# Optimization experiments

Measured on AMD Instinct MI355X. Metric: run time of the kernel, lower is better.

The kernel has to match this reference:

```python
import jax, jax.numpy as jnp
import numpy as np

D_MODEL = 512
HEADS = 8
FF_HIDDEN = 1024
EPS = 1e-6


def setup_inputs() -> dict:
    key = jax.random.key(0)
    ks = jax.random.split(key, 12)
    s = 1.0 / np.sqrt(D_MODEL)
    inp = {
        'x': jax.random.normal(ks[0], (2, 4096, D_MODEL), dtype=jnp.float32),
        'Wq': jax.random.normal(ks[1], (D_MODEL, D_MODEL), dtype=jnp.float32) * s,
        'bq': jnp.zeros((D_MODEL,), jnp.float32),
        'Wk': jax.random.normal(ks[2], (D_MODEL, D_MODEL), dtype=jnp.float32) * s,
        'bk': jnp.zeros((D_MODEL,), jnp.float32),
        'Wv': jax.random.normal(ks[3], (D_MODEL, D_MODEL), dtype=jnp.float32) * s,
        'bv': jnp.zeros((D_MODEL,), jnp.float32),
        'Wo': jax.random.normal(ks[4], (D_MODEL, D_MODEL), dtype=jnp.float32) * s,
        'bo': jnp.zeros((D_MODEL,), jnp.float32),
        'a1': jnp.ones((D_MODEL,), jnp.float32),
        'b1': jnp.zeros((D_MODEL,), jnp.float32),
        'a2': jnp.ones((D_MODEL,), jnp.float32),
        'b2': jnp.zeros((D_MODEL,), jnp.float32),
        'W1': jax.random.normal(ks[5], (D_MODEL, FF_HIDDEN), dtype=jnp.float32) * s,
        'c1': jnp.zeros((FF_HIDDEN,), jnp.float32),
        'W2': jax.random.normal(ks[6], (FF_HIDDEN, D_MODEL), dtype=jnp.float32) * (1.0 / np.sqrt(FF_HIDDEN)),
        'c2': jnp.zeros((D_MODEL,), jnp.float32),
    }
    return inp


def _layer_norm(x, a, b):
    # Faithful to source: uses unbiased std (torch default) and divides by (std + eps)
    mean = jnp.mean(x, axis=-1, keepdims=True)
    std = jnp.std(x, axis=-1, keepdims=True, ddof=1)
    return a * ((x - mean) / (std + EPS)) + b


def _encoder_block(x, Wq, bq, Wk, bk, Wv, bv, Wo, bo, a1, b1, a2, b2, W1, c1, W2, c2):
    B, S, D = x.shape
    H, dk = HEADS, D // HEADS
    q = (x @ Wq + bq).reshape(B, S, H, dk).transpose(0, 2, 1, 3)  # [B,H,S,dk]
    k = (x @ Wk + bk).reshape(B, S, H, dk).transpose(0, 2, 1, 3)
    v = (x @ Wv + bv).reshape(B, S, H, dk).transpose(0, 2, 1, 3)
    scores = jnp.einsum('bhqd,bhkd->bhqk', q, k) / np.sqrt(dk)
    probs = jax.nn.softmax(scores, axis=-1)
    attn = jnp.einsum('bhqk,bhkd->bhqd', probs, v)
    concat = attn.transpose(0, 2, 1, 3).reshape(B, S, D)
    attn_out = concat @ Wo + bo
    x = _layer_norm(x + attn_out, a1, b1)  # dropout = identity (eval mode)
    ffn = jax.nn.relu(x @ W1 + c1) @ W2 + c2
    return _layer_norm(x + ffn, a2, b2)


def reference(x, Wq, bq, Wk, bk, Wv, bv, Wo, bo, a1, b1, a2, b2, W1, c1, W2, c2):
    return _encoder_block(x, Wq, bq, Wk, bk, Wv, bv, Wo, bo, a1, b1, a2, b2, W1, c1, W2, c2)
```

## Files before the change

### kernel.cpp

```cpp
#include <hip/hip_runtime.h>
#include <stdint.h>

typedef short short8 __attribute__((ext_vector_type(8)));
typedef short short4v __attribute__((ext_vector_type(4)));
typedef float f32x4 __attribute__((ext_vector_type(4)));
typedef float f32x16 __attribute__((ext_vector_type(16)));
typedef unsigned int u32x4 __attribute__((ext_vector_type(4)));

#define LOG2E 1.44269504088896f
#define QSCALE (0.125f * LOG2E)

__device__ __forceinline__ unsigned short f2b(float f) {
  union { float f; unsigned int u; } x; x.f = f;
  unsigned int u = x.u;
  unsigned int r = (u + 0x7fffu + ((u >> 16) & 1u)) >> 16;
  return (unsigned short)r;
}
__device__ __forceinline__ float b2f(unsigned short s) {
  union { unsigned int u; float f; } x; x.u = ((unsigned int)s) << 16;
  return x.f;
}
__device__ __forceinline__ void gl16(const void* g, void* l) {
  __builtin_amdgcn_global_load_lds((const __attribute__((address_space(1))) void*)g,
                                   (__attribute__((address_space(3))) void*)l, 16, 0, 0);
}
__device__ __forceinline__ unsigned int cvtpk(float lo, float hi) {
  unsigned int r;
  asm("v_cvt_pk_bf16_f32 %0, %1, %2" : "=v"(r) : "v"(lo), "v"(hi));
  return r;
}
__device__ __forceinline__ void plswap(unsigned int& a, unsigned int& b) {
  asm volatile("v_permlane32_swap_b32 %0, %1" : "+v"(a), "+v"(b));
}

__global__ __launch_bounds__(256) void prep_k(
    const float* __restrict__ X, unsigned short* __restrict__ Xb,
    const float* __restrict__ Wq, const float* __restrict__ Wk,
    const float* __restrict__ Wv, const float* __restrict__ Wo,
    const float* __restrict__ W1, const float* __restrict__ W2,
    unsigned short* __restrict__ WqkvT, unsigned short* __restrict__ WoT,
    unsigned short* __restrict__ W1T, unsigned short* __restrict__ W2T,
    const float* __restrict__ bq, const float* __restrict__ bk,
    const float* __restrict__ bv, float* __restrict__ Bqkv) {
  __shared__ float t[64][65];
  int bid = blockIdx.x, tid = threadIdx.x;
  if (bid < 2048) {
    int i = bid * 256 + tid;
    const float* p = X + (size_t)i * 8;
    float4 a = *(const float4*)(p);
    float4 b = *(const float4*)(p + 4);
    short8 o;
    o[0] = (short)f2b(a.x); o[1] = (short)f2b(a.y);
    o[2] = (short)f2b(a.z); o[3] = (short)f2b(a.w);
    o[4] = (short)f2b(b.x); o[5] = (short)f2b(b.y);
    o[6] = (short)f2b(b.z); o[7] = (short)f2b(b.w);
    *(short8*)(Xb + (size_t)i * 8) = o;
    return;
  }
  if (bid == 2560) {
    for (int i = tid; i < 1536; i += 256) {
      float v = (i < 512) ? bq[i] * QSCALE : (i < 1024 ? bk[i - 512] : bv[i - 1024]);
      Bqkv[i] = v;
    }
    return;
  }
  int idx = bid - 2048;
  const float* W; unsigned short* WT; int K, N, kb, nb; float scale = 1.0f;
  if (idx < 256) {
    int sec = idx >> 6, local = idx & 63;
    K = 512; N = 512; kb = local >> 3; nb = local & 7;
    if (sec == 0) { W = Wq; WT = WqkvT; scale = QSCALE; }
    else if (sec == 1) { W = Wk; WT = WqkvT + 512 * 512; }
    else if (sec == 2) { W = Wv; WT = WqkvT + 2 * 512 * 512; }
    else { W = Wo; WT = WoT; }
  } else if (idx < 384) {
    int local = idx - 256; K = 512; N = 1024; kb = local >> 4; nb = local & 15;
    W = W1; WT = W1T;
  } else {
    int local = idx - 384; K = 1024; N = 512; kb = local >> 3; nb = local & 7;
    W = W2; WT = W2T;
  }
  int k0 = kb * 64, n0 = nb * 64;
  for (int i = tid; i < 4096; i += 256) {
    int r = i >> 6, c = i & 63;
    t[r][c] = W[(size_t)(k0 + r) * N + n0 + c];
  }
  __syncthreads();
  for (int i = tid; i < 4096; i += 256) {
    int r = i >> 6, c = i & 63;
    WT[(size_t)(n0 + r) * K + k0 + c] = f2b(t[c][r] * scale);
  }
}

template <int EPI>
__global__ __launch_bounds__(256) void gemm_bt(
    const unsigned short* __restrict__ A, const unsigned short* __restrict__ BT,
    const float* __restrict__ bias, float* __restrict__ Cf,
    unsigned short* __restrict__ Cb, int M, int N, int K) {
  __shared__ unsigned short As[128 * 32];
  __shared__ unsigned short Bs[128 * 32];
  int t = threadIdx.x, w = t >> 6, l = t & 63;
  int linb = blockIdx.x + gridDim.x * blockIdx.y;
  int q8 = (gridDim.x * gridDim.y) >> 3;
  int wk = (linb & 7) * q8 + (linb >> 3);
  int bm = wk / gridDim.y, bn = wk % gridDim.y;
  int wm = w >> 1, wn = w & 1;
  int g = l >> 4, ln = l & 15;
  f32x4 acc[4][4] = {};
  const unsigned short* Arow = A + (size_t)bm * 128 * K;
  const unsigned short* Brow = BT + (size_t)bn * 128 * K;
  int nk = K >> 5;
  for (int kt = 0; kt < nk; ++kt) {
    int k0 = kt * 32;
#pragma unroll
    for (int i = 0; i < 2; ++i) {
      int cl = i * 256 + t;
      int r = cl >> 2, c = cl & 3;
      char* ldsA = (char*)As + (size_t)(i * 256 + w * 64) * 16;
      char* ldsB = (char*)Bs + (size_t)(i * 256 + w * 64) * 16;
      gl16(Arow + (size_t)r * K + k0 + c * 8, ldsA);
      gl16(Brow + (size_t)r * K + k0 + c * 8, ldsB);
    }
    __syncthreads();
    short8 af[4], bf[4];
    int ko = g * 8;
#pragma unroll
    for (int i = 0; i < 4; ++i)
      af[i] = *(const short8*)&As[(wm * 64 + i * 16 + ln) * 32 + ko];
#pragma unroll
    for (int j = 0; j < 4; ++j)
      bf[j] = *(const short8*)&Bs[(wn * 64 + j * 16 + ln) * 32 + ko];
    __builtin_amdgcn_s_setprio(1);
#pragma unroll
    for (int i = 0; i < 4; ++i)
#pragma unroll
      for (int j = 0; j < 4; ++j)
        acc[i][j] = __builtin_amdgcn_mfma_f32_16x16x32_bf16(af[i], bf[j], acc[i][j], 0, 0, 0);
    __builtin_amdgcn_s_setprio(0);
    __syncthreads();
  }
#pragma unroll
  for (int i = 0; i < 4; ++i) {
    int row = bm * 128 + wm * 64 + i * 16 + g * 4;
#pragma unroll
    for (int j = 0; j < 4; ++j) {
      int col = bn * 128 + wn * 64 + j * 16 + ln;
      float bv = bias[col];
      float vv[4];
#pragma unroll
      for (int r = 0; r < 4; ++r) {
        float v = acc[i][j][r] + bv;
        if constexpr (EPI == 2) v = v > 0.f ? v : 0.f;
        vv[r] = v;
      }
      if constexpr (EPI == 3) {
        if (col < 1024) {
#pragma unroll
          for (int r = 0; r < 4; ++r)
            Cb[(size_t)(col >> 9) * 4194304 + (size_t)(row + r) * 512 + (col & 511)] = f2b(vv[r]);
        } else {
          short4v pk;
#pragma unroll
          for (int r = 0; r < 4; ++r) pk[r] = (short)f2b(vv[r]);
          *(short4v*)((unsigned short*)Cf +
                      (size_t)((row >> 12) * 512 + (col & 511)) * 4096 + (row & 4095)) = pk;
        }
      } else {
#pragma unroll
        for (int r = 0; r < 4; ++r)
          Cb[(size_t)(row + r) * N + col] = f2b(vv[r]);
      }
    }
  }
}

template <int AMODE, bool WB>
__global__ __launch_bounds__(512) void gemmln_k(
    const unsigned short* __restrict__ A, const unsigned short* __restrict__ BT,
    const float* __restrict__ bias, const float* __restrict__ X,
    const float* __restrict__ gamma, const float* __restrict__ beta,
    float* __restrict__ outf, unsigned short* __restrict__ outb,
    const unsigned short* __restrict__ Opart, const float* __restrict__ L,
    int K) {
  __shared__ unsigned short As[AMODE ? 32 * 520 : 32 * 32];
  __shared__ unsigned short Bs[512 * 32];
  __shared__ float stats[8][32][2];
  __shared__ float minv[32][2];
  __shared__ float sli[8][32];
  int tid = threadIdx.x, wv = tid >> 6, lane = tid & 63;
  int g = lane >> 4, ln = lane & 15;
  int bm = blockIdx.x;
  int row0 = bm * 32;
  f32x4 acc[2][4] = {};

  if constexpr (AMODE == 1) {
    int b = row0 >> 12;
    int q0 = row0 & 4095;
    if (tid < 256) {
      int h = tid >> 5, qq = tid & 31;
      int bh = b * 8 + h;
      float s = L[(size_t)bh * 4096 + q0 + qq] + L[(size_t)(16 + bh) * 4096 + q0 + qq];
      sli[h][qq] = 1.0f / s;
    }
    __syncthreads();
    int col = tid;
    int h = col >> 6, d = col & 63;
    int bh = b * 8 + h;
    const unsigned short* p0 = Opart + (size_t)bh * 262144 + (size_t)d * 4096 + q0;
    const unsigned short* p1 = Opart + (size_t)(16 + bh) * 262144 + (size_t)d * 4096 + q0;
#pragma unroll
    for (int i = 0; i < 4; ++i) {
      short8 a = *(const short8*)(p0 + i * 8);
      short8 c = *(const short8*)(p1 + i * 8);
#pragma unroll
      for (int j = 0; j < 8; ++j) {
        int qq = i * 8 + j;
        float s = (b2f((unsigned short)a[j]) + b2f((unsigned short)c[j])) * sli[h][qq];
        As[qq * 520 + col] = f2b(s);
      }
    }
    __syncthreads();
  }

  const unsigned short* Arow = (AMODE == 0) ? (A + (size_t)bm * 32 * K) : nullptr;
  int nk = K >> 5;
  for (int kt = 0; kt < nk; ++kt) {
    int k0 = kt * 32;
    if constexpr (AMODE == 0) {
      if (tid < 128) {
        int r = tid >> 2, c = tid & 3;
        gl16(Arow + (size_t)r * K + k0 + c * 8, (char*)As + tid * 16);
      }
    }
#pragma unroll
    for (int i = 0; i < 4; ++i) {
      int u = i * 512 + tid;
      int r = u >> 2, c = u & 3;
      gl16(BT + (size_t)r * K + k0 + c * 8, (char*)Bs + (size_t)u * 16);
    }
    __syncthreads();
    short8 af[2], bf[4];
#pragma unroll
    for (int i = 0; i < 2; ++i) {
      if constexpr (AMODE == 1)
        af[i] = *(const short8*)&As[(i * 16 + ln) * 520 + k0 + g * 8];
      else
        af[i] = *(const short8*)&As[(i * 16 + ln) * 32 + g * 8];
    }
#pragma unroll
    for (int j = 0; j < 4; ++j)
      bf[j] = *(const short8*)&Bs[(wv * 64 + j * 16 + ln) * 32 + g * 8];
    __builtin_amdgcn_s_setprio(1);
#pragma unroll
    for (int i = 0; i < 2; ++i)
#pragma unroll
      for (int j = 0; j < 4; ++j)
        acc[i][j] = __builtin_amdgcn_mfma_f32_16x16x32_bf16(af[i], bf[j], acc[i][j], 0, 0, 0);
    __builtin_amdgcn_s_setprio(0);
    __syncthreads();
  }
  float v[2][4][4];
  float ps[8], pss[8];
#pragma unroll
  for (int k = 0; k < 8; ++k) { ps[k] = 0.f; pss[k] = 0.f; }
#pragma unroll
  for (int i = 0; i < 2; ++i)
#pragma unroll
    for (int j = 0; j < 4; ++j) {
      int col = wv * 64 + j * 16 + ln;
      float bv = bias[col];
#pragma unroll
      for (int r = 0; r < 4; ++r) {
        int row = i * 16 + g * 4 + r;
        float t = acc[i][j][r] + bv + X[(size_t)(row0 + row) * 512 + col];
        v[i][j][r] = t;
        ps[i * 4 + r] += t; pss[i * 4 + r] += t * t;
      }
    }
#pragma unroll
  for (int off = 1; off < 16; off <<= 1) {
#pragma unroll
    for (int k = 0; k < 8; ++k) {
      ps[k] += __shfl_xor(ps[k], off);
      pss[k] += __shfl_xor(pss[k], off);
    }
  }
  if (ln == 0) {
#pragma unroll
    for (int i = 0; i < 2; ++i)
#pragma unroll
      for (int r = 0; r < 4; ++r) {
        stats[wv][i * 16 + g * 4 + r][0] = ps[i * 4 + r];
        stats[wv][i * 16 + g * 4 + r][1] = pss[i * 4 + r];
      }
  }
  __syncthreads();
  if (tid < 32) {
    float S = 0.f, SS = 0.f;
#pragma unroll
    for (int w2 = 0; w2 < 8; ++w2) { S += stats[w2][tid][0]; SS += stats[w2][tid][1]; }
    float mean = S * (1.f / 512.f);
    float var = fmaxf((SS - 512.f * mean * mean) * (1.f / 511.f), 0.f);
    minv[tid][0] = mean;
    minv[tid][1] = 1.f / (sqrtf(var) + 1e-6f);
  }
  __syncthreads();
#pragma unroll
  for (int i = 0; i < 2; ++i)
#pragma unroll
    for (int j = 0; j < 4; ++j) {
      int col = wv * 64 + j * 16 + ln;
      float gm = gamma[col], bt2 = beta[col];
#pragma unroll
      for (int r = 0; r < 4; ++r) {
        int row = i * 16 + g * 4 + r;
        float o = gm * ((v[i][j][r] - minv[row][0]) * minv[row][1]) + bt2;
        outf[(size_t)(row0 + row) * 512 + col] = o;
        if constexpr (WB) outb[(size_t)(row0 + row) * 512 + col] = f2b(o);
      }
    }
}

__global__ __launch_bounds__(256, 2) void attn_k(
    const unsigned short* __restrict__ Q, const unsigned short* __restrict__ Kb,
    const unsigned short* __restrict__ Vt, unsigned short* __restrict__ Opart,
    float* __restrict__ L) {
  __shared__ unsigned short Ks[2][4096];
  __shared__ unsigned short Vs[3][4096];
  int tid = threadIdx.x, wv = tid >> 6, lane = tid & 63;
  int l31 = lane & 31, hi = lane >> 5;
  int lin = blockIdx.x + 16 * blockIdx.y + 256 * blockIdx.z;
  int wk = (lin & 7) * 64 + (lin >> 3);
  int qb = wk & 15, bh = (wk >> 4) & 15, z = wk >> 8;
  int b = bh >> 3, h = bh & 7;
  int q0 = qb * 256 + wv * 64;
  int kvbase = z * 2048;

  short8 qfA[4], qfB[4];
  {
    const unsigned short* qpA = Q + (size_t)(b * 4096 + q0 + l31) * 512 + h * 64;
    const unsigned short* qpB = qpA + 32 * 512;
#pragma unroll
    for (int ks = 0; ks < 4; ++ks) {
      qfA[ks] = *(const short8*)(qpA + ks * 16 + hi * 8);
      qfB[ks] = *(const short8*)(qpB + ks * 16 + hi * 8);
    }
  }

  short8 ones;
#pragma unroll
  for (int j = 0; j < 8; ++j) ones[j] = (short)0x3F80;

  const f32x16 Z = {};
  f32x16 oA0 = {}, oA1 = {}, oB0 = {}, oB1 = {}, laccA = {}, laccB = {};

  int skk[2], sc[2];
#pragma unroll
  for (int i = 0; i < 2; ++i) {
    int u = i * 256 + tid;
    int r2 = u >> 4, s = u & 15;
    skk[i] = 2 * r2 + (s & 1);
    sc[i] = ((s >> 1) ^ (r2 & 7)) * 8;
  }

  auto stage = [&](char* kb_lds, char* vb_lds, int kv) {
    const unsigned short* ksrc = Kb + (size_t)(b * 4096 + kv) * 512 + h * 64;
    const unsigned short* vsrc = Vt + (size_t)(bh * 64) * 4096 + kv;
#pragma unroll
    for (int i = 0; i < 2; ++i) {
      gl16(ksrc + (size_t)skk[i] * 512 + sc[i], kb_lds + (size_t)(i * 256 + wv * 64) * 16);
      gl16(vsrc + (size_t)skk[i] * 4096 + sc[i], vb_lds + (size_t)(i * 256 + wv * 64) * 16);
    }
  };

  int r2a = l31 >> 1, par = l31 & 1, perm = r2a & 7;
  int rdb = r2a * 256 + (par << 4);

  auto qk = [&](const char* kbase, f32x16& sA0, f32x16& sA1, f32x16& sB0, f32x16& sB1) {
    __builtin_amdgcn_s_setprio(1);
#pragma unroll
    for (int ks = 0; ks < 4; ++ks) {
      int c16 = ks * 2 + hi;
      int byteA = rdb + (((c16 ^ perm) << 1) << 4);
      short8 k0 = *(const short8*)(kbase + byteA);
      short8 k1 = *(const short8*)(kbase + byteA + 4096);
      if (ks == 0) {
        sA0 = __builtin_amdgcn_mfma_f32_32x32x16_bf16(k0, qfA[0], Z, 0, 0, 0);
        sA1 = __builtin_amdgcn_mfma_f32_32x32x16_bf16(k1, qfA[0], Z, 0, 0, 0);
        sB0 = __builtin_amdgcn_mfma_f32_32x32x16_bf16(k0, qfB[0], Z, 0, 0, 0);
        sB1 = __builtin_amdgcn_mfma_f32_32x32x16_bf16(k1, qfB[0], Z, 0, 0, 0);
      } else {
        sA0 = __builtin_amdgcn_mfma_f32_32x32x16_bf16(k0, qfA[ks], sA0, 0, 0, 0);
        sA1 = __builtin_amdgcn_mfma_f32_32x32x16_bf16(k1, qfA[ks], sA1, 0, 0, 0);
        sB0 = __builtin_amdgcn_mfma_f32_32x32x16_bf16(k0, qfB[ks], sB0, 0, 0, 0);
        sB1 = __builtin_amdgcn_mfma_f32_32x32x16_bf16(k1, qfB[ks], sB1, 0, 0, 0);
      }
    }
    __builtin_amdgcn_s_setprio(0);
  };

  auto pv = [&](const char* vbase, const short8* pfA, const short8* pfB) {
    __builtin_amdgcn_s_setprio(1);
#pragma unroll
    for (int ks = 0; ks < 4; ++ks) {
      int c16 = ks * 2 + hi;
      int byteA = rdb + (((c16 ^ perm) << 1) << 4);
      short8 v0 = *(const short8*)(vbase + byteA);
      short8 v1 = *(const short8*)(vbase + byteA + 4096);
      oA0 = __builtin_amdgcn_mfma_f32_32x32x16_bf16(v0, pfA[ks], oA0, 0, 0, 0);
      oA1 = __builtin_amdgcn_mfma_f32_32x32x16_bf16(v1, pfA[ks], oA1, 0, 0, 0);
      oB0 = __builtin_amdgcn_mfma_f32_32x32x16_bf16(v0, pfB[ks], oB0, 0, 0, 0);
      oB1 = __builtin_amdgcn_mfma_f32_32x32x16_bf16(v1, pfB[ks], oB1, 0, 0, 0);
      laccA = __builtin_amdgcn_mfma_f32_32x32x16_bf16(ones, pfA[ks], laccA, 0, 0, 0);
      laccB = __builtin_amdgcn_mfma_f32_32x32x16_bf16(ones, pfB[ks], laccB, 0, 0, 0);
    }
    __builtin_amdgcn_s_setprio(0);
  };

  auto exppack = [&](f32x16& s0, f32x16& s1, short8* pf) {
#pragma unroll
    for (int r = 0; r < 16; ++r) s0[r] = __builtin_amdgcn_exp2f(s0[r]);
#pragma unroll
    for (int r = 0; r < 16; ++r) s1[r] = __builtin_amdgcn_exp2f(s1[r]);
    unsigned int u0 = cvtpk(s0[0], s0[1]), u1 = cvtpk(s0[4], s0[5]);
    plswap(u0, u1);
    unsigned int u2 = cvtpk(s0[2], s0[3]), u3 = cvtpk(s0[6], s0[7]);
    plswap(u2, u3);
    unsigned int u4 = cvtpk(s0[8], s0[9]), u5 = cvtpk(s0[12], s0[13]);
    plswap(u4, u5);
    unsigned int u6 = cvtpk(s0[10], s0[11]), u7 = cvtpk(s0[14], s0[15]);
    plswap(u6, u7);
    union { u32x4 u; short8 s; } cv;
    cv.u = (u32x4){u0, u2, u1, u3}; pf[0] = cv.s;
    cv.u = (u32x4){u4, u6, u5, u7}; pf[1] = cv.s;
    unsigned int w0 = cvtpk(s1[0], s1[1]), w1 = cvtpk(s1[4], s1[5]);
    plswap(w0, w1);
    unsigned int w2 = cvtpk(s1[2], s1[3]), w3 = cvtpk(s1[6], s1[7]);
    plswap(w2, w3);
    unsigned int w4 = cvtpk(s1[8], s1[9]), w5 = cvtpk(s1[12], s1[13]);
    plswap(w4, w5);
    unsigned int w6 = cvtpk(s1[10], s1[11]), w7 = cvtpk(s1[14], s1[15]);
    plswap(w6, w7);
    cv.u = (u32x4){w0, w2, w1, w3}; pf[2] = cv.s;
    cv.u = (u32x4){w4, w6, w5, w7}; pf[3] = cv.s;
  };

  char* k0b = (char*)&Ks[0][0];
  char* k1b = (char*)&Ks[1][0];
  char* vA = (char*)&Vs[0][0];
  char* vB = (char*)&Vs[1][0];
  char* vC = (char*)&Vs[2][0];
  stage(k0b, vA, kvbase);
  __syncthreads();
  stage(k1b, vB, kvbase + 64);

  f32x16 sA0, sA1, sB0, sB1;
  qk(k0b, sA0, sA1, sB0, sB1);
  short8 pfA[4], pfB[4];
  exppack(sA0, sA1, pfA);
  exppack(sB0, sB1, pfB);

#pragma unroll 1
  for (int t = 1; t < 32; ++t) {
    __syncthreads();
    char* kr = (t & 1) ? k1b : k0b;
    char* kw = (t & 1) ? k0b : k1b;
    if (t < 31) stage(kw, vC, kvbase + (t + 1) * 64);
    qk(kr, sA0, sA1, sB0, sB1);
    pv(vA, pfA, pfB);
    exppack(sA0, sA1, pfA);
    exppack(sB0, sB1, pfB);
    char* tmp = vA; vA = vB; vB = vC; vC = tmp;
  }
  pv(vA, pfA, pfB);

  int plane = z * 16 + bh;
  unsigned short* op = Opart + (size_t)plane * 262144;
  int qA = q0 + l31, qB = q0 + 32 + l31;
#pragma unroll
  for (int r = 0; r < 16; ++r) {
    int dr = (r & 3) + 8 * (r >> 2) + 4 * hi;
    op[(size_t)dr * 4096 + qA] = f2b(oA0[r]);
    op[(size_t)(dr + 32) * 4096 + qA] = f2b(oA1[r]);
    op[(size_t)dr * 4096 + qB] = f2b(oB0[r]);
    op[(size_t)(dr + 32) * 4096 + qB] = f2b(oB1[r]);
  }
  if (hi == 0) {
    L[(size_t)plane * 4096 + qA] = laccA[0];
    L[(size_t)plane * 4096 + qB] = laccB[0];
  }
}

extern "C" void kernel_launch(void* const* d_in, const int* in_sizes, int n_in,
                              void* d_out, int out_size, void* d_ws, size_t ws_size,
                              hipStream_t stream) {
  const float* x  = (const float*)d_in[0];
  const float* Wq = (const float*)d_in[1];
  const float* bq = (const float*)d_in[2];
  const float* Wk = (const float*)d_in[3];
  const float* bk = (const float*)d_in[4];
  const float* Wv = (const float*)d_in[5];
  const float* bv = (const float*)d_in[6];
  const float* Wo = (const float*)d_in[7];
  const float* bo = (const float*)d_in[8];
  const float* a1 = (const float*)d_in[9];
  const float* b1 = (const float*)d_in[10];
  const float* a2 = (const float*)d_in[11];
  const float* b2 = (const float*)d_in[12];
  const float* W1 = (const float*)d_in[13];
  const float* c1 = (const float*)d_in[14];
  const float* W2 = (const float*)d_in[15];
  const float* c2 = (const float*)d_in[16];

  char* ws = (char*)d_ws;
  const size_t MB = 1024 * 1024;
  unsigned short* Xb  = (unsigned short*)(ws + 0);
  unsigned short* Qb  = (unsigned short*)(ws + 8 * MB);
  unsigned short* Kbf = (unsigned short*)(ws + 16 * MB);
  float* L = (float*)(ws + 24 * MB);
  unsigned short* Vtb = (unsigned short*)(ws + 32 * MB);
  unsigned short* WqkvT = (unsigned short*)(ws + 40 * MB);
  unsigned short* WoT = (unsigned short*)(ws + 41 * MB + 512 * 1024);
  unsigned short* W1T = (unsigned short*)(ws + 42 * MB);
  unsigned short* W2T = (unsigned short*)(ws + 43 * MB);
  unsigned short* Opart = (unsigned short*)(ws + 44 * MB);
  float* Bqkv = (float*)(ws + 44 * MB);
  float* Y1 = (float*)(ws + 60 * MB);
  unsigned short* Y1b = Qb;
  unsigned short* Hb  = Kbf;

  prep_k<<<2561, 256, 0, stream>>>(x, Xb, Wq, Wk, Wv, Wo, W1, W2,
                                   WqkvT, WoT, W1T, W2T, bq, bk, bv, Bqkv);

  gemm_bt<3><<<dim3(64, 12), 256, 0, stream>>>(Xb, WqkvT, Bqkv, (float*)Vtb, Qb, 8192, 1536, 512);

  attn_k<<<dim3(16, 16, 2), 256, 0, stream>>>(Qb, Kbf, Vtb, Opart, L);

  gemmln_k<1, true><<<256, 512, 0, stream>>>(nullptr, WoT, bo, x, a1, b1, Y1, Y1b,
                                             Opart, L, 512);
  gemm_bt<2><<<dim3(64, 8), 256, 0, stream>>>(Y1b, W1T, c1, nullptr, Hb, 8192, 1024, 512);
  gemmln_k<0, false><<<256, 512, 0, stream>>>(Hb, W2T, c2, Y1, a2, b2, (float*)d_out, nullptr,
                                              nullptr, nullptr, 1024);
}
```

Measured before the change: 192.9 us.

## Double-buffer LDS tiles in GEMM kernels to overlap global loads with MFMA

Both the plain GEMM and the fused GEMM+LayerNorm kernels now use two LDS buffers, prefetching the next K tile with direct global-to-LDS loads while computing on the current one. Partial vmcnt waits replace full syncthreads so load latency can hide behind MFMA work. This doubles LDS use, which may lower occupancy, especially in the 512-thread LayerNorm kernel whose B tile grows to 64KB. The hand-counted vmcnt values must match the number of outstanding loads per wave.

```diff
diff --git a/kernel.cpp b/kernel.cpp
--- a/kernel.cpp
+++ b/kernel.cpp
@@ -97,8 +97,8 @@
     const unsigned short* __restrict__ A, const unsigned short* __restrict__ BT,
     const float* __restrict__ bias, float* __restrict__ Cf,
     unsigned short* __restrict__ Cb, int M, int N, int K) {
-  __shared__ unsigned short As[128 * 32];
-  __shared__ unsigned short Bs[128 * 32];
+  __shared__ unsigned short As[2][128 * 32];
+  __shared__ unsigned short Bs[2][128 * 32];
   int t = threadIdx.x, w = t >> 6, l = t & 63;
   int linb = blockIdx.x + gridDim.x * blockIdx.y;
   int q8 = (gridDim.x * gridDim.y) >> 3;
@@ -110,26 +110,39 @@
   const unsigned short* Arow = A + (size_t)bm * 128 * K;
   const unsigned short* Brow = BT + (size_t)bn * 128 * K;
   int nk = K >> 5;
-  for (int kt = 0; kt < nk; ++kt) {
+
+  auto stageg = [&](int buf, int kt) {
     int k0 = kt * 32;
 #pragma unroll
     for (int i = 0; i < 2; ++i) {
       int cl = i * 256 + t;
       int r = cl >> 2, c = cl & 3;
-      char* ldsA = (char*)As + (size_t)(i * 256 + w * 64) * 16;
-      char* ldsB = (char*)Bs + (size_t)(i * 256 + w * 64) * 16;
+      char* ldsA = (char*)&As[buf][0] + (size_t)(i * 256 + w * 64) * 16;
+      char* ldsB = (char*)&Bs[buf][0] + (size_t)(i * 256 + w * 64) * 16;
       gl16(Arow + (size_t)r * K + k0 + c * 8, ldsA);
       gl16(Brow + (size_t)r * K + k0 + c * 8, ldsB);
     }
-    __syncthreads();
+  };
+
+  stageg(0, 0);
+  for (int kt = 0; kt < nk; ++kt) {
+    int cur = kt & 1;
+    if (kt + 1 < nk) {
+      stageg(cur ^ 1, kt + 1);
+      asm volatile("s_waitcnt vmcnt(4)" ::: "memory");
+    } else {
+      asm volatile("s_waitcnt vmcnt(0)" ::: "memory");
+    }
+    __builtin_amdgcn_s_barrier();
+    __builtin_amdgcn_sched_barrier(0);
     short8 af[4], bf[4];
     int ko = g * 8;
 #pragma unroll
     for (int i = 0; i < 4; ++i)
-      af[i] = *(const short8*)&As[(wm * 64 + i * 16 + ln) * 32 + ko];
+      af[i] = *(const short8*)&As[cur][(wm * 64 + i * 16 + ln) * 32 + ko];
 #pragma unroll
     for (int j = 0; j < 4; ++j)
-      bf[j] = *(const short8*)&Bs[(wn * 64 + j * 16 + ln) * 32 + ko];
+      bf[j] = *(const short8*)&Bs[cur][(wn * 64 + j * 16 + ln) * 32 + ko];
     __builtin_amdgcn_s_setprio(1);
 #pragma unroll
     for (int i = 0; i < 4; ++i)
@@ -137,7 +150,7 @@
       for (int j = 0; j < 4; ++j)
         acc[i][j] = __builtin_amdgcn_mfma_f32_16x16x32_bf16(af[i], bf[j], acc[i][j], 0, 0, 0);
     __builtin_amdgcn_s_setprio(0);
-    __syncthreads();
+    __builtin_amdgcn_s_barrier();
   }
 #pragma unroll
   for (int i = 0; i < 4; ++i) {
@@ -182,8 +195,8 @@
     float* __restrict__ outf, unsigned short* __restrict__ outb,
     const unsigned short* __restrict__ Opart, const float* __restrict__ L,
     int K) {
-  __shared__ unsigned short As[AMODE ? 32 * 520 : 32 * 32];
-  __shared__ unsigned short Bs[512 * 32];
+  __shared__ unsigned short As[AMODE ? 32 * 520 : 2 * 32 * 32];
+  __shared__ unsigned short Bs[2][512 * 32];
   __shared__ float stats[8][32][2];
   __shared__ float minv[32][2];
   __shared__ float sli[8][32];
@@ -224,32 +237,51 @@
 
   const unsigned short* Arow = (AMODE == 0) ? (A + (size_t)bm * 32 * K) : nullptr;
   int nk = K >> 5;
-  for (int kt = 0; kt < nk; ++kt) {
+
+  auto stageg = [&](int buf, int kt) {
     int k0 = kt * 32;
     if constexpr (AMODE == 0) {
       if (tid < 128) {
         int r = tid >> 2, c = tid & 3;
-        gl16(Arow + (size_t)r * K + k0 + c * 8, (char*)As + tid * 16);
+        gl16(Arow + (size_t)r * K + k0 + c * 8, (char*)As + (size_t)buf * 2048 + tid * 16);
       }
     }
 #pragma unroll
     for (int i = 0; i < 4; ++i) {
       int u = i * 512 + tid;
       int r = u >> 2, c = u & 3;
-      gl16(BT + (size_t)r * K + k0 + c * 8, (char*)Bs + (size_t)u * 16);
-    }
-    __syncthreads();
+      gl16(BT + (size_t)r * K + k0 + c * 8, (char*)&Bs[buf][0] + (size_t)u * 16);
+    }
+  };
+
+  stageg(0, 0);
+  for (int kt = 0; kt < nk; ++kt) {
+    int cur = kt & 1;
+    if (kt + 1 < nk) {
+      stageg(cur ^ 1, kt + 1);
+      if constexpr (AMODE == 0) {
+        if (wv < 2) asm volatile("s_waitcnt vmcnt(5)" ::: "memory");
+        else        asm volatile("s_waitcnt vmcnt(4)" ::: "memory");
+      } else {
+        asm volatile("s_waitcnt vmcnt(4)" ::: "memory");
+      }
+    } else {
+      asm volatile("s_waitcnt vmcnt(0)" ::: "memory");
+    }
+    __builtin_amdgcn_s_barrier();
+    __builtin_amdgcn_sched_barrier(0);
+    int k0 = kt * 32;
     short8 af[2], bf[4];
 #pragma unroll
     for (int i = 0; i < 2; ++i) {
       if constexpr (AMODE == 1)
         af[i] = *(const short8*)&As[(i * 16 + ln) * 520 + k0 + g * 8];
       else
-        af[i] = *(const short8*)&As[(i * 16 + ln) * 32 + g * 8];
+        af[i] = *(const short8*)&As[cur * 1024 + (i * 16 + ln) * 32 + g * 8];
     }
 #pragma unroll
     for (int j = 0; j < 4; ++j)
-      bf[j] = *(const short8*)&Bs[(wv * 64 + j * 16 + ln) * 32 + g * 8];
+      bf[j] = *(const short8*)&Bs[cur][(wv * 64 + j * 16 + ln) * 32 + g * 8];
     __builtin_amdgcn_s_setprio(1);
 #pragma unroll
     for (int i = 0; i < 2; ++i)
@@ -257,7 +289,7 @@
       for (int j = 0; j < 4; ++j)
         acc[i][j] = __builtin_amdgcn_mfma_f32_16x16x32_bf16(af[i], bf[j], acc[i][j], 0, 0, 0);
     __builtin_amdgcn_s_setprio(0);
-    __syncthreads();
+    __builtin_amdgcn_s_barrier();
   }
   float v[2][4][4];
   float ps[8], pss[8];
```

After: 188.2 us, median of 2. 1.02x faster.
